# Optimization experiments

Measured on AMD Instinct MI355X. Metric: run time of the kernel, lower is better.

Reference implementation:

```python
import jax, jax.numpy as jnp
import numpy as np

N_SENTS, N_ENTS, BATCH, DIM, HEADS = 64, 16, 64, 512, 8


def setup_inputs() -> dict:
    key = jax.random.key(0)
    ks = jax.random.split(key, 10)
    se = N_SENTS * N_ENTS
    s = 0.02  # init scale for projection weights
    entities = jax.random.normal(ks[0], (se, BATCH, DIM), dtype=jnp.float32)
    query_param = jax.random.uniform(ks[1], (1, 1, DIM), jnp.float32, -1.0, 1.0)
    wq = jax.random.normal(ks[2], (DIM, DIM), jnp.float32) * s
    wk = jax.random.normal(ks[3], (DIM, DIM), jnp.float32) * s
    wv = jax.random.normal(ks[4], (DIM, DIM), jnp.float32) * s
    wo = jax.random.normal(ks[5], (DIM, DIM), jnp.float32) * s
    bq = jax.random.normal(ks[6], (DIM,), jnp.float32) * s
    bk = jax.random.normal(ks[7], (DIM,), jnp.float32) * s
    bv = jax.random.normal(ks[8], (DIM,), jnp.float32) * s
    bo = jax.random.normal(ks[9], (DIM,), jnp.float32) * s
    return {"entities": entities, "query_param": query_param,
            "wq": wq, "wk": wk, "wv": wv, "wo": wo,
            "bq": bq, "bk": bk, "bv": bv, "bo": bo,
            "n_sents": N_SENTS}


def reference(entities, query_param, wq, wk, wv, wo, bq, bk, bv, bo, n_sents):
    # entities: [n_sents*n_ents, batch, dim]
    se, b, d = entities.shape
    n_ents = se // n_sents
    h = HEADS
    hd = d // h

    # Learned single query broadcast to every (sentence, batch) slot.
    q_in = jnp.broadcast_to(query_param, (n_sents, b, d))
    q = q_in @ wq.T + bq            # [n_sents, b, d]
    k = entities @ wk.T + bk        # [se, b, d]
    v = entities @ wv.T + bv        # [se, b, d]

    # Split heads -> [b, h, len, hd]
    qh = q.reshape(n_sents, b, h, hd).transpose(1, 2, 0, 3)
    kh = k.reshape(se, b, h, hd).transpose(1, 2, 0, 3)
    vh = v.reshape(se, b, h, hd).transpose(1, 2, 0, 3)

    scale = jnp.asarray(1.0 / np.sqrt(hd), dtype=qh.dtype)
    scores = jnp.einsum('bhqd,bhkd->bhqk', qh, kh) * scale  # [b,h,n_sents,se]

    # Block-diagonal mask: query i attends only to keys [i*n_ents, (i+1)*n_ents)
    valid = (jnp.arange(se) // n_ents)[None, :] == jnp.arange(n_sents)[:, None]
    scores = jnp.where(valid[None, None], scores, jnp.finfo(scores.dtype).min)

    attn = jax.nn.softmax(scores, axis=-1)
    ctx = jnp.einsum('bhqk,bhkd->bhqd', attn, vh)            # [b,h,n_sents,hd]
    out = ctx.transpose(2, 0, 1, 3).reshape(n_sents, b, d)   # merge heads
    return out @ wo.T + bo                                   # [n_sents, b, d]
```

## Files before the change

kernel.cpp:

```cpp
#include <hip/hip_runtime.h>
#include <stdint.h>

#define HEADS 8
#define DIM   512
#define HD    64
#define NE    16
#define NS    64
#define NB    64

typedef short bf16x8 __attribute__((ext_vector_type(8)));
typedef float f32x4  __attribute__((ext_vector_type(4)));

__device__ __forceinline__ unsigned short f2bf(float f) {
    union { float f; uint32_t u; } v; v.f = f;
    uint32_t u = v.u;
    u += 0x7fffu + ((u >> 16) & 1u);
    return (unsigned short)(u >> 16);
}
__device__ __forceinline__ float bf_lo(uint32_t u) {
    union { uint32_t u; float f; } v; v.u = u << 16; return v.f;
}
__device__ __forceinline__ float bf_hi(uint32_t u) {
    union { uint32_t u; float f; } v; v.u = u & 0xffff0000u; return v.f;
}

__device__ __forceinline__ uint32_t cvt2(float a, float b) {
    uint32_t r;
    asm("v_cvt_pk_bf16_f32 %0, %1, %2" : "=v"(r) : "v"(a), "v"(b));
    return r;
}
__device__ __forceinline__ uint2 cvt4(float4 v) {
    return (uint2){cvt2(v.x, v.y), cvt2(v.z, v.w)};
}

__global__ __launch_bounds__(256) void k_prep(
    const float* __restrict__ qp, const float* __restrict__ wq,
    const float* __restrict__ bq, const float* __restrict__ wk,
    const float* __restrict__ wv, const float* __restrict__ wo,
    unsigned short* __restrict__ u_bf,
    unsigned short* __restrict__ wv_bf, unsigned short* __restrict__ wo_bf)
{
    const int bid = blockIdx.x;
    const int t = threadIdx.x;
    if (bid < 16) {
        const int h = bid >> 1, ch = bid & 1;
        __shared__ float qs[HD];
        {
            const int j = t >> 2, q = t & 3;
            const float* w = wq + (size_t)(h * HD + j) * DIM + q * 128;
            const float* qq = qp + q * 128;
            float a = 0.f;
            #pragma unroll 8
            for (int i = 0; i < 128; i++) a += w[i] * qq[i];
            a += __shfl_xor(a, 1);
            a += __shfl_xor(a, 2);
            if (q == 0) qs[j] = a + bq[h * HD + j];
        }
        __syncthreads();
        const int c = ch * 256 + t;
        const float* w = wk + (size_t)(h * HD) * DIM + c;
        float acc = 0.f;
        #pragma unroll 8
        for (int j = 0; j < HD; j++) acc += qs[j] * w[(size_t)j * DIM];
        u_bf[h * DIM + c] = f2bf(acc);
        u_bf[(h + 8) * DIM + c] = 0;
        return;
    }
    const bool is_v = bid < 272;
    const float* src = is_v ? wv : wo;
    unsigned short* dst = is_v ? wv_bf : wo_bf;
    const int li = ((is_v ? bid - 16 : bid - 272) * 1024 + t * 4);
    const float4 v = *(const float4*)(src + li);
    ushort4 hv;
    hv.x = f2bf(v.x); hv.y = f2bf(v.y); hv.z = f2bf(v.z); hv.w = f2bf(v.w);
    *(ushort4*)(dst + li) = hv;
}

__global__ __launch_bounds__(256, 8) void k_attn(
    const float* __restrict__ ents, const unsigned short* __restrict__ u_bf,
    unsigned short* __restrict__ weighted)
{
    __shared__ unsigned short ent[NE * DIM];
    __shared__ float attn_s[NE][8];
    const int t = threadIdx.x;
    const int bid = blockIdx.x;
    const int s = bid >> 6, b = bid & 63;

    {
        const float* base = ents + ((size_t)(s * NE) * NB + b) * DIM;
        #pragma unroll
        for (int i = 0; i < 8; i++) {
            const int c = t + 256 * i;
            const int e = c >> 7, d4 = c & 127;
            const float4 v = *(const float4*)(base + (size_t)e * (NB * DIM) + (d4 << 2));
            const uint2 hv = cvt4(v);
            const uint32_t off = (uint32_t)((e << 10) | (d4 << 3)) ^ (uint32_t)((e & 7) << 4);
            *(uint2*)((char*)ent + off) = hv;
        }
    }
    __syncthreads();

    if (t < 64) {
        const int m = t & 15, g = t >> 4;
        const uint32_t swz = (uint32_t)((m & 7) << 4);
        const uint32_t rowb = (uint32_t)(m << 10);
        const unsigned short* urow = u_bf + m * DIM + g * 8;
        f32x4 acc = {0.f, 0.f, 0.f, 0.f};
        #pragma unroll
        for (int ks = 0; ks < 16; ks++) {
            const int kp = g * 8 + ks * 32;
            const bf16x8 af = *(const bf16x8*)((const char*)ent + ((rowb + (uint32_t)(kp << 1)) ^ swz));
            const bf16x8 bf = *(const bf16x8*)(urow + ks * 32);
            acc = __builtin_amdgcn_mfma_f32_16x16x32_bf16(af, bf, acc, 0, 0, 0);
        }
        const float scale = 0.125f;
        float s0 = acc[0]*scale, s1 = acc[1]*scale, s2 = acc[2]*scale, s3 = acc[3]*scale;
        float mx = fmaxf(fmaxf(s0, s1), fmaxf(s2, s3));
        mx = fmaxf(mx, __shfl_xor(mx, 16));
        mx = fmaxf(mx, __shfl_xor(mx, 32));
        const float p0 = __expf(s0 - mx), p1 = __expf(s1 - mx);
        const float p2 = __expf(s2 - mx), p3 = __expf(s3 - mx);
        float sm = p0 + p1 + p2 + p3;
        sm += __shfl_xor(sm, 16);
        sm += __shfl_xor(sm, 32);
        const float inv = 1.f / sm;
        if (m < HEADS) {
            attn_s[4 * g + 0][m] = p0 * inv;
            attn_s[4 * g + 1][m] = p1 * inv;
            attn_s[4 * g + 2][m] = p2 * inv;
            attn_s[4 * g + 3][m] = p3 * inv;
        }
    }
    __syncthreads();

    {
        const int d0 = t << 1;
        unsigned short* wrow = weighted + ((size_t)bid << 12) + d0;
        #pragma unroll
        for (int hp = 0; hp < 2; hp++) {
            float accx[4], accy[4];
            #pragma unroll
            for (int h = 0; h < 4; h++) { accx[h] = 0.f; accy[h] = 0.f; }
            #pragma unroll
            for (int e = 0; e < NE; e++) {
                const uint32_t off = (uint32_t)((e << 10) | (d0 << 1)) ^ (uint32_t)((e & 7) << 4);
                const uint32_t rv = *(const uint32_t*)((const char*)ent + off);
                const float ev0 = bf_lo(rv), ev1 = bf_hi(rv);
                const f32x4 a = *(const f32x4*)&attn_s[e][hp * 4];
                accx[0] += a.x * ev0; accy[0] += a.x * ev1;
                accx[1] += a.y * ev0; accy[1] += a.y * ev1;
                accx[2] += a.z * ev0; accy[2] += a.z * ev1;
                accx[3] += a.w * ev0; accy[3] += a.w * ev1;
            }
            #pragma unroll
            for (int h = 0; h < 4; h++) {
                *(uint32_t*)(wrow + (hp * 4 + h) * DIM) = cvt2(accx[h], accy[h]);
            }
        }
    }
}

template <typename CT>
__global__ __launch_bounds__(256) void k_gemm(
    const unsigned short* __restrict__ A, int lda, int aOffY,
    const unsigned short* __restrict__ B, int ldb, int bOffY,
    const float* __restrict__ bias, CT* __restrict__ C, int ldc, int cOffY, int K)
{
    __shared__ unsigned short a_s[64][72];
    __shared__ unsigned short b_s[64][72];
    const int t = threadIdx.x;
    const int m0 = blockIdx.x * 64;
    const int y  = blockIdx.y;
    const int w = t >> 6, l = t & 63;
    const int m = l & 15, g = l >> 4;
    const int lr = t >> 2, lk = (t & 3) * 16;

    const unsigned short* Ap = A + (size_t)(m0 + lr) * lda + (size_t)aOffY * y;
    const unsigned short* Bp = B + (size_t)(bOffY * y + lr) * ldb;

    f32x4 acc[4];
    #pragma unroll
    for (int i = 0; i < 4; i++) acc[i] = (f32x4){0.f, 0.f, 0.f, 0.f};

    for (int k0 = 0; k0 < K; k0 += 64) {
        const ushort4 av0 = *(const ushort4*)(Ap + k0 + lk);
        const ushort4 av1 = *(const ushort4*)(Ap + k0 + lk + 4);
        const ushort4 av2 = *(const ushort4*)(Ap + k0 + lk + 8);
        const ushort4 av3 = *(const ushort4*)(Ap + k0 + lk + 12);
        const ushort4 bv0 = *(const ushort4*)(Bp + k0 + lk);
        const ushort4 bv1 = *(const ushort4*)(Bp + k0 + lk + 4);
        const ushort4 bv2 = *(const ushort4*)(Bp + k0 + lk + 8);
        const ushort4 bv3 = *(const ushort4*)(Bp + k0 + lk + 12);
        *(ushort4*)&a_s[lr][lk]      = av0;
        *(ushort4*)&a_s[lr][lk + 4]  = av1;
        *(ushort4*)&a_s[lr][lk + 8]  = av2;
        *(ushort4*)&a_s[lr][lk + 12] = av3;
        *(ushort4*)&b_s[lr][lk]      = bv0;
        *(ushort4*)&b_s[lr][lk + 4]  = bv1;
        *(ushort4*)&b_s[lr][lk + 8]  = bv2;
        *(ushort4*)&b_s[lr][lk + 12] = bv3;
        __syncthreads();
        #pragma unroll
        for (int kk = 0; kk < 64; kk += 32) {
            const int kp = kk + g * 8;
            const bf16x8 af = *(const bf16x8*)&a_s[w * 16 + m][kp];
            const bf16x8 b0 = *(const bf16x8*)&b_s[ 0 + m][kp];
            const bf16x8 b1 = *(const bf16x8*)&b_s[16 + m][kp];
            const bf16x8 b2 = *(const bf16x8*)&b_s[32 + m][kp];
            const bf16x8 b3 = *(const bf16x8*)&b_s[48 + m][kp];
            acc[0] = __builtin_amdgcn_mfma_f32_16x16x32_bf16(af, b0, acc[0], 0, 0, 0);
            acc[1] = __builtin_amdgcn_mfma_f32_16x16x32_bf16(af, b1, acc[1], 0, 0, 0);
            acc[2] = __builtin_amdgcn_mfma_f32_16x16x32_bf16(af, b2, acc[2], 0, 0, 0);
            acc[3] = __builtin_amdgcn_mfma_f32_16x16x32_bf16(af, b3, acc[3], 0, 0, 0);
        }
        __syncthreads();
    }

    const int colbase = cOffY * y;
    #pragma unroll
    for (int nt = 0; nt < 4; nt++) {
        const int col = colbase + nt * 16 + m;
        const float bs = bias[col];
        #pragma unroll
        for (int j = 0; j < 4; j++) {
            const int row = m0 + w * 16 + g * 4 + j;
            const float val = acc[nt][j] + bs;
            if (sizeof(CT) == 2) {
                ((unsigned short*)C)[(size_t)row * ldc + col] = f2bf(val);
            } else {
                ((float*)C)[(size_t)row * ldc + col] = val;
            }
        }
    }
}

extern "C" void kernel_launch(void* const* d_in, const int* in_sizes, int n_in,
                              void* d_out, int out_size, void* d_ws, size_t ws_size,
                              hipStream_t stream)
{
    const float* ents = (const float*)d_in[0];
    const float* qp   = (const float*)d_in[1];
    const float* wq   = (const float*)d_in[2];
    const float* wk   = (const float*)d_in[3];
    const float* wv   = (const float*)d_in[4];
    const float* wo   = (const float*)d_in[5];
    const float* bq   = (const float*)d_in[6];
    const float* bv   = (const float*)d_in[8];
    const float* bo   = (const float*)d_in[9];

    char* ws = (char*)d_ws;
    unsigned short* u_bf     = (unsigned short*)ws;
    unsigned short* wv_bf    = (unsigned short*)(ws + 65536);
    unsigned short* wo_bf    = (unsigned short*)(ws + 65536 + 524288);
    unsigned short* weighted = (unsigned short*)(ws + 2097152);
    unsigned short* ctx      = (unsigned short*)(ws + 2097152 + 33554432);

    k_prep <<<528, 256, 0, stream>>>(qp, wq, bq, wk, wv, wo, u_bf, wv_bf, wo_bf);
    k_attn <<<4096, 256, 0, stream>>>(ents, u_bf, weighted);
    k_gemm<unsigned short><<<dim3(64, 8), 256, 0, stream>>>(
        weighted, HEADS * DIM, DIM, wv_bf, DIM, HD, bv, ctx, DIM, HD, DIM);
    k_gemm<float><<<dim3(64, 8), 256, 0, stream>>>(
        ctx, DIM, 0, wo_bf, DIM, HD, bo, (float*)d_out, DIM, HD, DIM);
}
```

Baseline: 62.11 us.

## Fuse V-projection and output-projection GEMMs into one kernel with LDS-resident ctx

Replaces the two separate GEMM launches (weighted×Wv → ctx, ctx×Wo → out) with one kernel. Each 512-thread block loads 16 rows of the weighted tensor into swizzled LDS, computes ctx into LDS, then applies Wo and writes fp32 output. This drops a launch and the global round-trip of the ctx intermediate. In exchange it uses only 256 blocks at one block per CU with about 144KB of LDS, and B operands are read straight from global memory with no LDS staging, which may limit occupancy and load efficiency.

```diff
diff --git a/kernel.cpp b/kernel.cpp
--- a/kernel.cpp
+++ b/kernel.cpp
@@ -160,75 +160,87 @@
     }
 }
 
-template <typename CT>
-__global__ __launch_bounds__(256) void k_gemm(
-    const unsigned short* __restrict__ A, int lda, int aOffY,
-    const unsigned short* __restrict__ B, int ldb, int bOffY,
-    const float* __restrict__ bias, CT* __restrict__ C, int ldc, int cOffY, int K)
-{
-    __shared__ unsigned short a_s[64][72];
-    __shared__ unsigned short b_s[64][72];
+__global__ __launch_bounds__(512, 1) void k_out(
+    const unsigned short* __restrict__ weighted,
+    const unsigned short* __restrict__ wv_bf,
+    const unsigned short* __restrict__ wo_bf,
+    const float* __restrict__ bv, const float* __restrict__ bo,
+    float* __restrict__ out)
+{
+    __shared__ unsigned short a_s[16 * 4096];
+    __shared__ unsigned short ctx_s[16 * 512];
     const int t = threadIdx.x;
-    const int m0 = blockIdx.x * 64;
-    const int y  = blockIdx.y;
-    const int w = t >> 6, l = t & 63;
-    const int m = l & 15, g = l >> 4;
-    const int lr = t >> 2, lk = (t & 3) * 16;
-
-    const unsigned short* Ap = A + (size_t)(m0 + lr) * lda + (size_t)aOffY * y;
-    const unsigned short* Bp = B + (size_t)(bOffY * y + lr) * ldb;
-
-    f32x4 acc[4];
-    #pragma unroll
-    for (int i = 0; i < 4; i++) acc[i] = (f32x4){0.f, 0.f, 0.f, 0.f};
-
-    for (int k0 = 0; k0 < K; k0 += 64) {
-        const ushort4 av0 = *(const ushort4*)(Ap + k0 + lk);
-        const ushort4 av1 = *(const ushort4*)(Ap + k0 + lk + 4);
-        const ushort4 av2 = *(const ushort4*)(Ap + k0 + lk + 8);
-        const ushort4 av3 = *(const ushort4*)(Ap + k0 + lk + 12);
-        const ushort4 bv0 = *(const ushort4*)(Bp + k0 + lk);
-        const ushort4 bv1 = *(const ushort4*)(Bp + k0 + lk + 4);
-        const ushort4 bv2 = *(const ushort4*)(Bp + k0 + lk + 8);
-        const ushort4 bv3 = *(const ushort4*)(Bp + k0 + lk + 12);
-        *(ushort4*)&a_s[lr][lk]      = av0;
-        *(ushort4*)&a_s[lr][lk + 4]  = av1;
-        *(ushort4*)&a_s[lr][lk + 8]  = av2;
-        *(ushort4*)&a_s[lr][lk + 12] = av3;
-        *(ushort4*)&b_s[lr][lk]      = bv0;
-        *(ushort4*)&b_s[lr][lk + 4]  = bv1;
-        *(ushort4*)&b_s[lr][lk + 8]  = bv2;
-        *(ushort4*)&b_s[lr][lk + 12] = bv3;
-        __syncthreads();
-        #pragma unroll
-        for (int kk = 0; kk < 64; kk += 32) {
-            const int kp = kk + g * 8;
-            const bf16x8 af = *(const bf16x8*)&a_s[w * 16 + m][kp];
-            const bf16x8 b0 = *(const bf16x8*)&b_s[ 0 + m][kp];
-            const bf16x8 b1 = *(const bf16x8*)&b_s[16 + m][kp];
-            const bf16x8 b2 = *(const bf16x8*)&b_s[32 + m][kp];
-            const bf16x8 b3 = *(const bf16x8*)&b_s[48 + m][kp];
-            acc[0] = __builtin_amdgcn_mfma_f32_16x16x32_bf16(af, b0, acc[0], 0, 0, 0);
-            acc[1] = __builtin_amdgcn_mfma_f32_16x16x32_bf16(af, b1, acc[1], 0, 0, 0);
-            acc[2] = __builtin_amdgcn_mfma_f32_16x16x32_bf16(af, b2, acc[2], 0, 0, 0);
-            acc[3] = __builtin_amdgcn_mfma_f32_16x16x32_bf16(af, b3, acc[3], 0, 0, 0);
-        }
-        __syncthreads();
-    }
-
-    const int colbase = cOffY * y;
-    #pragma unroll
-    for (int nt = 0; nt < 4; nt++) {
-        const int col = colbase + nt * 16 + m;
-        const float bs = bias[col];
-        #pragma unroll
-        for (int j = 0; j < 4; j++) {
-            const int row = m0 + w * 16 + g * 4 + j;
-            const float val = acc[nt][j] + bs;
-            if (sizeof(CT) == 2) {
-                ((unsigned short*)C)[(size_t)row * ldc + col] = f2bf(val);
-            } else {
-                ((float*)C)[(size_t)row * ldc + col] = val;
+    const int w = t >> 6, lane = t & 63;
+    const int m = lane & 15, g = lane >> 4;
+    const int sb0 = blockIdx.x * 16;
+
+    {
+        const int r = t >> 5, c = t & 31;
+        const unsigned short* src = weighted + ((size_t)(sb0 + r) << 12) + c * 8;
+        const uint32_t swz = (uint32_t)((r & 7) << 4);
+        #pragma unroll
+        for (int i = 0; i < 16; i++) {
+            const uint4 v = *(const uint4*)(src + i * 256);
+            const uint32_t off = ((uint32_t)((r << 13) | (i << 9) | (c << 4))) ^ swz;
+            *(uint4*)((char*)a_s + off) = v;
+        }
+    }
+    __syncthreads();
+
+    {
+        const uint32_t aswz = (uint32_t)((m & 7) << 4);
+        f32x4 acc[4];
+        #pragma unroll
+        for (int ct = 0; ct < 4; ct++) acc[ct] = (f32x4){0.f, 0.f, 0.f, 0.f};
+        #pragma unroll
+        for (int ks = 0; ks < 16; ks++) {
+            const int k = g * 8 + ks * 32;
+            const bf16x8 af = *(const bf16x8*)((const char*)a_s +
+                (((uint32_t)((m << 13) | (w << 10) | (k << 1))) ^ aswz));
+            #pragma unroll
+            for (int ct = 0; ct < 4; ct++) {
+                const bf16x8 bf = *(const bf16x8*)(wv_bf + (size_t)((w * 64 + ct * 16 + m) << 9) + k);
+                acc[ct] = __builtin_amdgcn_mfma_f32_16x16x32_bf16(af, bf, acc[ct], 0, 0, 0);
+            }
+        }
+        #pragma unroll
+        for (int ct = 0; ct < 4; ct++) {
+            const int col = w * 64 + ct * 16 + m;
+            const float bb = bv[col];
+            #pragma unroll
+            for (int j = 0; j < 4; j++) {
+                const int r = 4 * g + j;
+                const uint32_t off = ((uint32_t)((r << 10) | (col << 1))) ^ (uint32_t)((r & 7) << 4);
+                *(unsigned short*)((char*)ctx_s + off) = f2bf(acc[ct][j] + bb);
+            }
+        }
+    }
+    __syncthreads();
+
+    {
+        const uint32_t cswz = (uint32_t)((m & 7) << 4);
+        f32x4 acc[4];
+        #pragma unroll
+        for (int ct = 0; ct < 4; ct++) acc[ct] = (f32x4){0.f, 0.f, 0.f, 0.f};
+        #pragma unroll
+        for (int ks = 0; ks < 16; ks++) {
+            const int k = g * 8 + ks * 32;
+            const bf16x8 af = *(const bf16x8*)((const char*)ctx_s +
+                (((uint32_t)((m << 10) | (k << 1))) ^ cswz));
+            #pragma unroll
+            for (int ct = 0; ct < 4; ct++) {
+                const bf16x8 bf = *(const bf16x8*)(wo_bf + (size_t)((w * 64 + ct * 16 + m) << 9) + k);
+                acc[ct] = __builtin_amdgcn_mfma_f32_16x16x32_bf16(af, bf, acc[ct], 0, 0, 0);
+            }
+        }
+        #pragma unroll
+        for (int ct = 0; ct < 4; ct++) {
+            const int col = w * 64 + ct * 16 + m;
+            const float bb = bo[col];
+            #pragma unroll
+            for (int j = 0; j < 4; j++) {
+                const int row = sb0 + 4 * g + j;
+                out[(size_t)(row << 9) + col] = acc[ct][j] + bb;
             }
         }
     }
@@ -253,12 +265,8 @@
     unsigned short* wv_bf    = (unsigned short*)(ws + 65536);
     unsigned short* wo_bf    = (unsigned short*)(ws + 65536 + 524288);
     unsigned short* weighted = (unsigned short*)(ws + 2097152);
-    unsigned short* ctx      = (unsigned short*)(ws + 2097152 + 33554432);
 
     k_prep <<<528, 256, 0, stream>>>(qp, wq, bq, wk, wv, wo, u_bf, wv_bf, wo_bf);
     k_attn <<<4096, 256, 0, stream>>>(ents, u_bf, weighted);
-    k_gemm<unsigned short><<<dim3(64, 8), 256, 0, stream>>>(
-        weighted, HEADS * DIM, DIM, wv_bf, DIM, HD, bv, ctx, DIM, HD, DIM);
-    k_gemm<float><<<dim3(64, 8), 256, 0, stream>>>(
-        ctx, DIM, 0, wo_bf, DIM, HD, bo, (float*)d_out, DIM, HD, DIM);
-}
+    k_out  <<<256, 512, 0, stream>>>(weighted, wv_bf, wo_bf, bv, bo, (float*)d_out);
+}
```

New measurement: 79.20 us. +27.5%, slower.

## Load entity tiles via direct global-to-LDS DMA in fp32 with swizzle

Applied to the files above, without the earlier changes.

The attention kernel now stages entity rows with global_load_lds straight into LDS as fp32, using an XOR swizzle on the source index, rather than loading into registers, converting to bf16 and storing. Conversion to bf16 moves to the MFMA score loop, and the weighted-sum loop reads fp32 directly. The aim is to skip the register round trip and conversion on the load path. In exchange, LDS per block doubles, occupancy drops (launch bound 8 to 4), and the score path does extra conversion work.

```diff
diff --git a/kernel.cpp b/kernel.cpp
--- a/kernel.cpp
+++ b/kernel.cpp
@@ -17,12 +17,6 @@
     u += 0x7fffu + ((u >> 16) & 1u);
     return (unsigned short)(u >> 16);
 }
-__device__ __forceinline__ float bf_lo(uint32_t u) {
-    union { uint32_t u; float f; } v; v.u = u << 16; return v.f;
-}
-__device__ __forceinline__ float bf_hi(uint32_t u) {
-    union { uint32_t u; float f; } v; v.u = u & 0xffff0000u; return v.f;
-}
 
 __device__ __forceinline__ uint32_t cvt2(float a, float b) {
     uint32_t r;
@@ -31,6 +25,12 @@
 }
 __device__ __forceinline__ uint2 cvt4(float4 v) {
     return (uint2){cvt2(v.x, v.y), cvt2(v.z, v.w)};
+}
+__device__ __forceinline__ bf16x8 cvt8(float4 lo, float4 hi) {
+    union { uint32_t u[4]; bf16x8 v; } r;
+    r.u[0] = cvt2(lo.x, lo.y); r.u[1] = cvt2(lo.z, lo.w);
+    r.u[2] = cvt2(hi.x, hi.y); r.u[3] = cvt2(hi.z, hi.w);
+    return r.v;
 }
 
 __global__ __launch_bounds__(256) void k_prep(
@@ -76,13 +76,14 @@
     *(ushort4*)(dst + li) = hv;
 }
 
-__global__ __launch_bounds__(256, 8) void k_attn(
+__global__ __launch_bounds__(256, 4) void k_attn(
     const float* __restrict__ ents, const unsigned short* __restrict__ u_bf,
     unsigned short* __restrict__ weighted)
 {
-    __shared__ unsigned short ent[NE * DIM];
+    __shared__ float ent_f[NE * DIM];
     __shared__ float attn_s[NE][8];
     const int t = threadIdx.x;
+    const int w = t >> 6, lane = t & 63;
     const int bid = blockIdx.x;
     const int s = bid >> 6, b = bid & 63;
 
@@ -90,26 +91,30 @@
         const float* base = ents + ((size_t)(s * NE) * NB + b) * DIM;
         #pragma unroll
         for (int i = 0; i < 8; i++) {
-            const int c = t + 256 * i;
-            const int e = c >> 7, d4 = c & 127;
-            const float4 v = *(const float4*)(base + (size_t)e * (NB * DIM) + (d4 << 2));
-            const uint2 hv = cvt4(v);
-            const uint32_t off = (uint32_t)((e << 10) | (d4 << 3)) ^ (uint32_t)((e & 7) << 4);
-            *(uint2*)((char*)ent + off) = hv;
+            const int p  = ((w * 8 + i) << 6) | lane;
+            const int e  = p >> 7;
+            const int jp = p & 127;
+            const int j  = jp ^ (e & 7);
+            const float* src = base + (size_t)e * (NB * DIM) + (j << 2);
+            float* dst = ent_f + ((w * 8 + i) << 8);
+            __builtin_amdgcn_global_load_lds(
+                (const __attribute__((address_space(1))) void*)src,
+                (__attribute__((address_space(3))) void*)dst, 16, 0, 0);
         }
     }
     __syncthreads();
 
     if (t < 64) {
         const int m = t & 15, g = t >> 4;
-        const uint32_t swz = (uint32_t)((m & 7) << 4);
-        const uint32_t rowb = (uint32_t)(m << 10);
+        const int esw = m & 7;
         const unsigned short* urow = u_bf + m * DIM + g * 8;
         f32x4 acc = {0.f, 0.f, 0.f, 0.f};
         #pragma unroll
         for (int ks = 0; ks < 16; ks++) {
-            const int kp = g * 8 + ks * 32;
-            const bf16x8 af = *(const bf16x8*)((const char*)ent + ((rowb + (uint32_t)(kp << 1)) ^ swz));
+            const int j0 = g * 2 + ks * 8;
+            const float4 f0 = *(const float4*)&ent_f[(m << 9) + (( j0      ^ esw) << 2)];
+            const float4 f1 = *(const float4*)&ent_f[(m << 9) + (((j0 + 1) ^ esw) << 2)];
+            const bf16x8 af = cvt8(f0, f1);
             const bf16x8 bf = *(const bf16x8*)(urow + ks * 32);
             acc = __builtin_amdgcn_mfma_f32_16x16x32_bf16(af, bf, acc, 0, 0, 0);
         }
@@ -134,8 +139,8 @@
     __syncthreads();
 
     {
-        const int d0 = t << 1;
-        unsigned short* wrow = weighted + ((size_t)bid << 12) + d0;
+        const int jg = t >> 1, hf = t & 1;
+        unsigned short* wrow = weighted + ((size_t)bid << 12) + (t << 1);
         #pragma unroll
         for (int hp = 0; hp < 2; hp++) {
             float accx[4], accy[4];
@@ -143,14 +148,12 @@
             for (int h = 0; h < 4; h++) { accx[h] = 0.f; accy[h] = 0.f; }
             #pragma unroll
             for (int e = 0; e < NE; e++) {
-                const uint32_t off = (uint32_t)((e << 10) | (d0 << 1)) ^ (uint32_t)((e & 7) << 4);
-                const uint32_t rv = *(const uint32_t*)((const char*)ent + off);
-                const float ev0 = bf_lo(rv), ev1 = bf_hi(rv);
+                const float2 ev = *(const float2*)&ent_f[(e << 9) + ((jg ^ (e & 7)) << 2) + (hf << 1)];
                 const f32x4 a = *(const f32x4*)&attn_s[e][hp * 4];
-                accx[0] += a.x * ev0; accy[0] += a.x * ev1;
-                accx[1] += a.y * ev0; accy[1] += a.y * ev1;
-                accx[2] += a.z * ev0; accy[2] += a.z * ev1;
-                accx[3] += a.w * ev0; accy[3] += a.w * ev1;
+                accx[0] += a.x * ev.x; accy[0] += a.x * ev.y;
+                accx[1] += a.y * ev.x; accy[1] += a.y * ev.y;
+                accx[2] += a.z * ev.x; accy[2] += a.z * ev.y;
+                accx[3] += a.w * ev.x; accy[3] += a.w * ev.y;
             }
             #pragma unroll
             for (int h = 0; h < 4; h++) {
```

Measured after the change: 64.69 us. +4.2%, slower.
